# Optimization experiments

Measured on AMD Instinct MI355X. Metric: run time of the kernel, lower is better.

## Reference

```python
import jax, jax.numpy as jnp
import numpy as np

B, S, D, H, L, FF = 32, 512, 256, 8, 2, 512
E = 64  # embed_dim_per_feature
VOCABS = [20, 50, 100]
NCLS = 36
MAX_CONN, THR = 10, 0.6


def _ln(x, g, b, eps=1e-5):
    m = x.mean(-1, keepdims=True)
    v = ((x - m) ** 2).mean(-1, keepdims=True)
    return g * (x - m) / jnp.sqrt(v + eps) + b


def _build_adj(cat, cnt):
    # self loops + chain links + banded similarity links (create_mutation_graph_optimized)
    Bb, _, Ss = cat.shape
    adj = jnp.broadcast_to(jnp.eye(Ss, dtype=jnp.float32), (Bb, Ss, Ss))
    for d in range(1, MAX_CONN):
        if d >= Ss:
            break
        cat_sim = (cat[:, :, :-d] == cat[:, :, d:]).astype(jnp.float32).mean(1)
        cnt_sim = jnp.exp(-jnp.abs(cnt[:, :-d] - cnt[:, d:]) / 100.0)
        sim = 0.5 * (cat_sim + cnt_sim)  # [B, S-d]
        base = 1.0 if d == 1 else 0.0  # chain link stays 1 when sim<=thr
        val = jnp.where(sim > THR, sim, base)
        ii = jnp.arange(Ss - d)
        adj = adj.at[:, ii, ii + d].set(val)
        adj = adj.at[:, ii + d, ii].set(val)
    return adj


def setup_inputs():
    key = jax.random.key(0)
    ks = iter(jax.random.split(key, 40))
    def nrm(shape, s=0.02):
        return jax.random.normal(next(ks), shape, jnp.float32) * s
    return {
        "categorical_x": jax.random.randint(next(ks), (B, 3, S), 0, min(VOCABS)),
        "count_x": jax.random.uniform(next(ks), (B, S), jnp.float32) * 100.0,
        "emb0": nrm((VOCABS[0], E)), "emb1": nrm((VOCABS[1], E)), "emb2": nrm((VOCABS[2], E)),
        "cnt_W": nrm((1, E)), "cnt_b": jnp.zeros((E,), jnp.float32),
        "pos_enc": nrm((S, D)),
        "gat_W": nrm((L, D, D)), "gat_a": nrm((L, 2 * D, 1)),
        "qkv_W": nrm((L, 3 * D, D)), "qkv_b": jnp.zeros((L, 3 * D), jnp.float32),
        "outp_W": nrm((L, D, D)), "outp_b": jnp.zeros((L, D), jnp.float32),
        "ff1_W": nrm((L, FF, D)), "ff1_b": jnp.zeros((L, FF), jnp.float32),
        "ff2_W": nrm((L, D, FF)), "ff2_b": jnp.zeros((L, D), jnp.float32),
        "ln_g": jnp.ones((L, 3, D), jnp.float32), "ln_b": jnp.zeros((L, 3, D), jnp.float32),
        "cls1_W": nrm((D // 2, D)), "cls1_b": jnp.zeros((D // 2,), jnp.float32),
        "cls2_W": nrm((NCLS, D // 2)), "cls2_b": jnp.zeros((NCLS,), jnp.float32),
    }


def reference(categorical_x, count_x, emb0, emb1, emb2, cnt_W, cnt_b, pos_enc,
              gat_W, gat_a, qkv_W, qkv_b, outp_W, outp_b,
              ff1_W, ff1_b, ff2_W, ff2_b, ln_g, ln_b,
              cls1_W, cls1_b, cls2_W, cls2_b):
    Ss = categorical_x.shape[2]
    # per-timestep feature embedding + count projection, concat -> d_model
    x = jnp.concatenate([
        emb0[categorical_x[:, 0]], emb1[categorical_x[:, 1]], emb2[categorical_x[:, 2]],
        count_x[..., None] @ cnt_W + cnt_b], -1)
    x = x + pos_enc[:Ss]
    mask = _build_adj(categorical_x, count_x) > 0  # adj used only as mask
    dh = D // H
    for l in range(L):
        # GraphAttentionLayer: e_ij = Wh_i.a1 + Wh_j.a2 (same math as repeat+concat+matmul)
        Wh = x @ gat_W[l]
        e = (Wh @ gat_a[l][:D, 0])[:, :, None] + (Wh @ gat_a[l][D:, 0])[:, None, :]
        att = jax.nn.softmax(jnp.where(mask, e, -9e15), -1)
        g = jax.nn.elu(att @ Wh)
        x = _ln(x + g, ln_g[l, 0], ln_b[l, 0])
        # MultiheadAttention (batch_first, eval)
        qkv = x @ qkv_W[l].T + qkv_b[l]
        q, k, v = jnp.split(qkv, 3, -1)
        q = q.reshape(-1, Ss, H, dh)
        k = k.reshape(-1, Ss, H, dh)
        v = v.reshape(-1, Ss, H, dh)
        sc = jnp.einsum('bihd,bjhd->bhij', q, k) / jnp.sqrt(jnp.float32(dh))
        o = jnp.einsum('bhij,bjhd->bihd', jax.nn.softmax(sc, -1), v).reshape(-1, Ss, D)
        o = o @ outp_W[l].T + outp_b[l]
        x = _ln(x + o, ln_g[l, 1], ln_b[l, 1])
        # FFN
        ff = jax.nn.relu(x @ ff1_W[l].T + ff1_b[l]) @ ff2_W[l].T + ff2_b[l]
        x = _ln(x + ff, ln_g[l, 2], ln_b[l, 2])
    pooled = x.mean(1)
    h = jax.nn.relu(pooled @ cls1_W.T + cls1_b)
    return h @ cls2_W.T + cls2_b
```

## Files before the change

### kernel.cpp

```cpp
#include <hip/hip_runtime.h>
#include <hip/hip_bf16.h>
#include <math.h>

#define Bn 32
#define Sn 512
#define Dn 256
#define Hn 8
#define DHn 32
#define En 64
#define FFn 512
#define Ln 2
#define NCLSn 36
#define BANDR 9
#define NBn 19
#define Mn (Bn * Sn)

typedef __attribute__((ext_vector_type(8))) short s8v;
typedef __attribute__((ext_vector_type(4))) float f4v;
typedef __attribute__((ext_vector_type(4))) unsigned short us4;
typedef unsigned short ushortT;

__device__ __forceinline__ ushortT f2b(float f) {
    unsigned u = __float_as_uint(f);
    unsigned r = (u + 0x7FFFu + ((u >> 16) & 1u)) >> 16;
    return (ushortT)r;
}

#define GLDS16(g, l)                                                            \
    __builtin_amdgcn_global_load_lds(                                           \
        (const __attribute__((address_space(1))) void*)(g),                     \
        (__attribute__((address_space(3))) void*)(l), 16, 0, 0)

__global__ void k_f2b_all(const float* __restrict__ qkvW, const float* __restrict__ outpW,
                          const float* __restrict__ ff1W, const float* __restrict__ ff2W,
                          const float* __restrict__ gatW,
                          ushortT* __restrict__ qkvWb, ushortT* __restrict__ outpWb,
                          ushortT* __restrict__ ff1Wb, ushortT* __restrict__ ff2Wb,
                          ushortT* __restrict__ gatWb) {
    int bid = blockIdx.x;
    if (bid < 1024) {
        int i4 = bid * 256 + threadIdx.x;
        const float* src; ushortT* dst; int off;
        if (i4 < 98304)       { src = qkvW;  dst = qkvWb;  off = 0; }
        else if (i4 < 131072) { src = outpW; dst = outpWb; off = 98304; }
        else if (i4 < 196608) { src = ff1W;  dst = ff1Wb;  off = 131072; }
        else                  { src = ff2W;  dst = ff2Wb;  off = 196608; }
        int j = (i4 - off) * 4;
        float4 v = *(const float4*)(src + j);
        us4 o = {f2b(v.x), f2b(v.y), f2b(v.z), f2b(v.w)};
        *(us4*)(dst + j) = o;
    } else {
        int i = (bid - 1024) * 256 + threadIdx.x;
        int l = i >> 16, rem = i & 65535;
        int k = rem >> 8, n = rem & 255;
        gatWb[(l << 16) + n * 256 + k] = f2b(gatW[i]);
    }
}

__global__ void k_embed_mask(const int* __restrict__ cat, const float* __restrict__ cnt,
                             const float* __restrict__ e0, const float* __restrict__ e1,
                             const float* __restrict__ e2,
                             const float* __restrict__ cW, const float* __restrict__ cb,
                             const float* __restrict__ pos, float* __restrict__ x,
                             ushortT* __restrict__ xb, unsigned char* __restrict__ maskp) {
    if (blockIdx.x < Mn) {
        int bs = blockIdx.x;
        int d = threadIdx.x;
        int b = bs >> 9, s = bs & 511;
        float v;
        if (d < 64)       v = e0[cat[(b * 3 + 0) * Sn + s] * En + d];
        else if (d < 128) v = e1[cat[(b * 3 + 1) * Sn + s] * En + (d - 64)];
        else if (d < 192) v = e2[cat[(b * 3 + 2) * Sn + s] * En + (d - 128)];
        else              v = cnt[b * Sn + s] * cW[d - 192] + cb[d - 192];
        float y = v + pos[s * Dn + d];
        x[(size_t)bs * Dn + d] = y;
        xb[(size_t)bs * Dn + d] = f2b(y);
    } else {
        int idx = (blockIdx.x - Mn) * 256 + threadIdx.x;
        if (idx >= Bn * Sn * NBn) return;
        int off = idx % NBn;
        int bs = idx / NBn;
        int b = bs >> 9, i = bs & 511;
        int j = i + off - BANDR;
        unsigned char m = 0;
        if (j >= 0 && j < Sn) {
            int dd = off - BANDR;
            int ad = dd < 0 ? -dd : dd;
            if (ad <= 1) {
                m = 1;
            } else {
                int c = 0;
                for (int f = 0; f < 3; f++)
                    c += (cat[(b * 3 + f) * Sn + i] == cat[(b * 3 + f) * Sn + j]);
                float cat_sim = (float)c / 3.0f;
                float cnt_sim = expf(-fabsf(cnt[b * Sn + i] - cnt[b * Sn + j]) / 100.0f);
                float sim = 0.5f * (cat_sim + cnt_sim);
                m = (sim > 0.6f) ? 1 : 0;
            }
        }
        maskp[idx] = m;
    }
}

template <int ACT>
__global__ __launch_bounds__(256) void k_gemm_mfma(const ushortT* __restrict__ A,
                                                   const ushortT* __restrict__ Bt,
                                                   const float* __restrict__ bias,
                                                   ushortT* __restrict__ Cout,
                                                   int M, int N, int K) {
    __shared__ ushortT As[2][128 * 32];
    __shared__ ushortT Bs[2][128 * 32];
    int tid = threadIdx.x;
    int w = tid >> 6, lane = tid & 63;
    int g = lane >> 4, lr = lane & 15;
    int o_ = blockIdx.y * gridDim.x + blockIdx.x;
    int nwg = gridDim.x * gridDim.y;
    int wid = (o_ & 7) * (nwg >> 3) + (o_ >> 3);
    int m0 = (wid / gridDim.x) * 128, n0 = (wid % gridDim.x) * 128;
    int wr = w >> 1, wc = w & 1;
    int NT = K >> 5;
    f4v acc[4][4];
#pragma unroll
    for (int m = 0; m < 4; m++)
#pragma unroll
        for (int n = 0; n < 4; n++) acc[m][n] = (f4v){0.f, 0.f, 0.f, 0.f};

    auto stage = [&](int t, int buf) {
        int k0 = t << 5;
#pragma unroll
        for (int r = 0; r < 2; r++) {
            int e = (tid + r * 256) * 8;
            int row = e >> 5, kk = e & 31;
            GLDS16(A + (size_t)(m0 + row) * K + k0 + kk, &As[buf][e]);
            GLDS16(Bt + (size_t)(n0 + row) * K + k0 + kk, &Bs[buf][e]);
        }
    };

    stage(0, 0);
    __syncthreads();
    for (int t = 0; t < NT; t++) {
        int cur = t & 1;
        if (t + 1 < NT) stage(t + 1, cur ^ 1);
        s8v af[4], bf[4];
#pragma unroll
        for (int m = 0; m < 4; m++)
            af[m] = *(const s8v*)(&As[cur][(wr * 64 + m * 16 + lr) * 32 + g * 8]);
#pragma unroll
        for (int n = 0; n < 4; n++)
            bf[n] = *(const s8v*)(&Bs[cur][(wc * 64 + n * 16 + lr) * 32 + g * 8]);
#pragma unroll
        for (int m = 0; m < 4; m++)
#pragma unroll
            for (int n = 0; n < 4; n++)
                acc[m][n] = __builtin_amdgcn_mfma_f32_16x16x32_bf16(af[m], bf[n], acc[m][n], 0, 0, 0);
        __syncthreads();
    }
#pragma unroll
    for (int m = 0; m < 4; m++) {
#pragma unroll
        for (int n = 0; n < 4; n++) {
            int col = n0 + wc * 64 + n * 16 + lr;
            float bv = bias ? bias[col] : 0.0f;
#pragma unroll
            for (int r = 0; r < 4; r++) {
                int row = m0 + wr * 64 + m * 16 + g * 4 + r;
                float v = acc[m][n][r] + bv;
                if (ACT == 1) v = fmaxf(v, 0.0f);
                Cout[(size_t)row * N + col] = f2b(v);
            }
        }
    }
}

template <int MODE>
__global__ __launch_bounds__(512) void k_gemm_row(const ushortT* __restrict__ A,
                                                  const ushortT* __restrict__ Bt,
                                                  const float* __restrict__ bias,
                                                  const float* __restrict__ ga,
                                                  float* __restrict__ a1h, float* __restrict__ a2h,
                                                  float* __restrict__ Whout,
                                                  const float* __restrict__ lg,
                                                  const float* __restrict__ lb,
                                                  float* __restrict__ x, ushortT* __restrict__ xb,
                                                  int K) {
    __shared__ ushortT As[2][64 * 32];
    __shared__ ushortT Bs[2][256 * 32];
    __shared__ float red1[64][4], red2[64][4];
    int tid = threadIdx.x;
    int w = tid >> 6, lane = tid & 63;
    int g = lane >> 4, lr = lane & 15;
    int wr = w >> 2, wc = w & 3;
    int o_ = blockIdx.x;
    int wid = (o_ & 7) * (gridDim.x >> 3) + (o_ >> 3);
    int m0 = wid * 64;
    int NT = K >> 5;
    f4v acc[2][4];
#pragma unroll
    for (int m = 0; m < 2; m++)
#pragma unroll
        for (int n = 0; n < 4; n++) acc[m][n] = (f4v){0.f, 0.f, 0.f, 0.f};

    auto stage = [&](int t, int buf) {
        int k0 = t << 5;
        if (tid < 256) {
            int e = tid * 8;
            int row = e >> 5, kk = e & 31;
            GLDS16(A + (size_t)(m0 + row) * K + k0 + kk, &As[buf][e]);
        }
#pragma unroll
        for (int r = 0; r < 2; r++) {
            int e = (tid + r * 512) * 8;
            int row = e >> 5, kk = e & 31;
            GLDS16(Bt + (size_t)row * K + k0 + kk, &Bs[buf][e]);
        }
    };

    stage(0, 0);
    __syncthreads();
    for (int t = 0; t < NT; t++) {
        int cur = t & 1;
        if (t + 1 < NT) stage(t + 1, cur ^ 1);
        s8v af[2], bf[4];
#pragma unroll
        for (int m = 0; m < 2; m++)
            af[m] = *(const s8v*)(&As[cur][(wr * 32 + m * 16 + lr) * 32 + g * 8]);
#pragma unroll
        for (int n = 0; n < 4; n++)
            bf[n] = *(const s8v*)(&Bs[cur][(wc * 64 + n * 16 + lr) * 32 + g * 8]);
#pragma unroll
        for (int m = 0; m < 2; m++)
#pragma unroll
            for (int n = 0; n < 4; n++)
                acc[m][n] = __builtin_amdgcn_mfma_f32_16x16x32_bf16(af[m], bf[n], acc[m][n], 0, 0, 0);
        __syncthreads();
    }

    int cn[4];
#pragma unroll
    for (int n = 0; n < 4; n++) cn[n] = wc * 64 + n * 16 + lr;

    if constexpr (MODE == 0) {
        float a1v[4], a2v[4];
#pragma unroll
        for (int n = 0; n < 4; n++) { a1v[n] = ga[cn[n]]; a2v[n] = ga[Dn + cn[n]]; }
#pragma unroll
        for (int m = 0; m < 2; m++)
#pragma unroll
            for (int r = 0; r < 4; r++) {
                int rowl = wr * 32 + m * 16 + g * 4 + r;
                float p1 = 0.f, p2 = 0.f;
#pragma unroll
                for (int n = 0; n < 4; n++) {
                    float v = acc[m][n][r];
                    Whout[(size_t)(m0 + rowl) * Dn + cn[n]] = v;
                    p1 += v * a1v[n];
                    p2 += v * a2v[n];
                }
                p1 += __shfl_xor(p1, 1); p2 += __shfl_xor(p2, 1);
                p1 += __shfl_xor(p1, 2); p2 += __shfl_xor(p2, 2);
                p1 += __shfl_xor(p1, 4); p2 += __shfl_xor(p2, 4);
                p1 += __shfl_xor(p1, 8); p2 += __shfl_xor(p2, 8);
                if (lr == 0) { red1[rowl][wc] = p1; red2[rowl][wc] = p2; }
            }
        __syncthreads();
        if (tid < 64) {
            float t1 = red1[tid][0] + red1[tid][1] + red1[tid][2] + red1[tid][3];
            float t2 = red2[tid][0] + red2[tid][1] + red2[tid][2] + red2[tid][3];
            a1h[m0 + tid] = t1;
            a2h[m0 + tid] = t2;
        }
    } else {
        float bv[4], lgv[4], lbv[4];
#pragma unroll
        for (int n = 0; n < 4; n++) { bv[n] = bias[cn[n]]; lgv[n] = lg[cn[n]]; lbv[n] = lb[cn[n]]; }
#pragma unroll
        for (int m = 0; m < 2; m++)
#pragma unroll
            for (int r = 0; r < 4; r++) {
                int rowl = wr * 32 + m * 16 + g * 4 + r;
                float s1 = 0.f, s2 = 0.f;
#pragma unroll
                for (int n = 0; n < 4; n++) {
                    float y = acc[m][n][r] + bv[n] + x[(size_t)(m0 + rowl) * Dn + cn[n]];
                    acc[m][n][r] = y;
                    s1 += y;
                    s2 += y * y;
                }
                s1 += __shfl_xor(s1, 1); s2 += __shfl_xor(s2, 1);
                s1 += __shfl_xor(s1, 2); s2 += __shfl_xor(s2, 2);
                s1 += __shfl_xor(s1, 4); s2 += __shfl_xor(s2, 4);
                s1 += __shfl_xor(s1, 8); s2 += __shfl_xor(s2, 8);
                if (lr == 0) { red1[rowl][wc] = s1; red2[rowl][wc] = s2; }
            }
        __syncthreads();
#pragma unroll
        for (int m = 0; m < 2; m++)
#pragma unroll
            for (int r = 0; r < 4; r++) {
                int rowl = wr * 32 + m * 16 + g * 4 + r;
                float S1 = red1[rowl][0] + red1[rowl][1] + red1[rowl][2] + red1[rowl][3];
                float S2 = red2[rowl][0] + red2[rowl][1] + red2[rowl][2] + red2[rowl][3];
                float mean = S1 * (1.0f / Dn);
                float var = S2 * (1.0f / Dn) - mean * mean;
                float rs = rsqrtf(var + 1e-5f);
#pragma unroll
                for (int n = 0; n < 4; n++) {
                    float o = lgv[n] * (acc[m][n][r] - mean) * rs + lbv[n];
                    size_t idx = (size_t)(m0 + rowl) * Dn + cn[n];
                    x[idx] = o;
                    xb[idx] = f2b(o);
                }
            }
    }
}

__global__ __launch_bounds__(256) void k_gat_attn_ln(const float* __restrict__ Wh,
                                                     const float* __restrict__ a1h,
                                                     const float* __restrict__ a2h,
                                                     const unsigned char* __restrict__ mask,
                                                     const float* __restrict__ lg,
                                                     const float* __restrict__ lb,
                                                     float* __restrict__ x,
                                                     ushortT* __restrict__ xb) {
    int w = threadIdx.x >> 6, l = threadIdx.x & 63;
    int bs = blockIdx.x * 4 + w;
    int b = bs >> 9, i = bs & 511;
    float e = -1e30f;
    int j = i + l - BANDR;
    if (l < NBn && j >= 0 && j < Sn && mask[bs * NBn + l])
        e = a1h[bs] + a2h[(b << 9) + j];
    float mx = e;
#pragma unroll
    for (int o = 32; o; o >>= 1) mx = fmaxf(mx, __shfl_xor(mx, o));
    float p = (e > -1e29f) ? __expf(e - mx) : 0.0f;
    float sum = p;
#pragma unroll
    for (int o = 32; o; o >>= 1) sum += __shfl_xor(sum, o);
    p *= (1.0f / sum);
    int c4 = l * 4;
    const float* whb = Wh + (size_t)(b << 9) * Dn + c4;
    float gx = 0.f, gy = 0.f, gz = 0.f, gw = 0.f;
#pragma unroll
    for (int o = 0; o < NBn; o++) {
        float wo = __shfl(p, o);
        int jo = i + o - BANDR;
        jo = jo < 0 ? 0 : (jo > Sn - 1 ? Sn - 1 : jo);
        float4 v = *(const float4*)(whb + (size_t)jo * Dn);
        gx += wo * v.x; gy += wo * v.y; gz += wo * v.z; gw += wo * v.w;
    }
    gx = gx > 0.f ? gx : expm1f(gx);
    gy = gy > 0.f ? gy : expm1f(gy);
    gz = gz > 0.f ? gz : expm1f(gz);
    gw = gw > 0.f ? gw : expm1f(gw);
    float4 xv = *(const float4*)(x + (size_t)bs * Dn + c4);
    float y0 = xv.x + gx, y1 = xv.y + gy, y2 = xv.z + gz, y3 = xv.w + gw;
    float s1 = y0 + y1 + y2 + y3;
    float s2 = y0 * y0 + y1 * y1 + y2 * y2 + y3 * y3;
#pragma unroll
    for (int o = 32; o; o >>= 1) {
        s1 += __shfl_xor(s1, o);
        s2 += __shfl_xor(s2, o);
    }
    float mean = s1 * (1.0f / Dn);
    float var = s2 * (1.0f / Dn) - mean * mean;
    float r = rsqrtf(var + 1e-5f);
    float4 lgv = *(const float4*)(lg + c4);
    float4 lbv = *(const float4*)(lb + c4);
    float o0 = lgv.x * (y0 - mean) * r + lbv.x;
    float o1 = lgv.y * (y1 - mean) * r + lbv.y;
    float o2 = lgv.z * (y2 - mean) * r + lbv.z;
    float o3 = lgv.w * (y3 - mean) * r + lbv.w;
    *(float4*)(x + (size_t)bs * Dn + c4) = make_float4(o0, o1, o2, o3);
    us4 ob = {f2b(o0), f2b(o1), f2b(o2), f2b(o3)};
    *(us4*)(xb + (size_t)bs * Dn + c4) = ob;
}

__global__ __launch_bounds__(256) void k_attn_mfma(const ushortT* __restrict__ qkv,
                                                   ushortT* __restrict__ ob) {
    __shared__ ushortT Ks[2][64 * 32];
    __shared__ ushortT Vt[2][32 * 64];
    __shared__ ushortT Ps[4][32 * 72];
    int tid = threadIdx.x;
    int w = tid >> 6, lane = tid & 63;
    int g = lane >> 4, lr = lane & 15;
    int o_ = blockIdx.x;
    int blk = (o_ & 7) * (gridDim.x >> 3) + (o_ >> 3);
    int qq = blk & 3, h = (blk >> 2) & 7, b = blk >> 5;
    const ushortT* base = qkv + (size_t)b * Sn * 768;
    const ushortT* kbase = base + 256 + h * 32;
    const ushortT* vbase = base + 512 + h * 32;

    int krow2 = tid >> 3;
    int kc = (tid & 7) ^ (krow2 & 7);
    int kkv = krow2 * 2 + (kc >> 2);
    int kdd = (kc & 3) * 8;
    int vd0 = w * 8;

    int q0 = qq * 128 + w * 32;
    s8v qf[2];
#pragma unroll
    for (int m = 0; m < 2; m++)
        qf[m] = *(const s8v*)(base + (size_t)(q0 + m * 16 + lr) * 768 + h * 32 + g * 8);

    f4v o[2][2];
    float rl[2][4];
#pragma unroll
    for (int m = 0; m < 2; m++) {
        o[m][0] = (f4v){0.f, 0.f, 0.f, 0.f};
        o[m][1] = (f4v){0.f, 0.f, 0.f, 0.f};
#pragma unroll
        for (int r = 0; r < 4; r++) rl[m][r] = 0.f;
    }
    const float scale2 = 0.25506973f;

    {
        GLDS16(kbase + (size_t)kkv * 768 + kdd, &Ks[0][tid * 8]);
        us4 v0 = *(const us4*)(vbase + (size_t)lane * 768 + vd0);
        us4 v1 = *(const us4*)(vbase + (size_t)lane * 768 + vd0 + 4);
#pragma unroll
        for (int jj = 0; jj < 4; jj++) {
            int d = vd0 + jj;
            Vt[0][d * 64 + (lane ^ ((d & 7) << 3))] = v0[jj];
            int d2 = d + 4;
            Vt[0][d2 * 64 + (lane ^ ((d2 & 7) << 3))] = v1[jj];
        }
    }
    __syncthreads();

    for (int kt = 0; kt < 8; kt++) {
        int cur = kt & 1, nxt = cur ^ 1;
        us4 v0, v1;
        if (kt < 7) {
            GLDS16(kbase + (size_t)((kt + 1) * 64 + kkv) * 768 + kdd, &Ks[nxt][tid * 8]);
            v0 = *(const us4*)(vbase + (size_t)((kt + 1) * 64 + lane) * 768 + vd0);
            v1 = *(const us4*)(vbase + (size_t)((kt + 1) * 64 + lane) * 768 + vd0 + 4);
        }
        s8v kf[4];
#pragma unroll
        for (int n = 0; n < 4; n++) {
            int row2 = n * 8 + (lr >> 1);
            int cc = (((lr & 1) << 2) + g) ^ (row2 & 7);
            kf[n] = *(const s8v*)(&Ks[cur][row2 * 64 + cc * 8]);
        }
        s8v vf[2][2];
#pragma unroll
        for (int cd = 0; cd < 2; cd++)
#pragma unroll
            for (int c2 = 0; c2 < 2; c2++) {
                int d = cd * 16 + lr;
                vf[cd][c2] = *(const s8v*)(&Vt[cur][d * 64 + ((c2 * 32 + g * 8) ^ ((d & 7) << 3))]);
            }
        f4v s[2][4];
#pragma unroll
        for (int m = 0; m < 2; m++)
#pragma unroll
            for (int n = 0; n < 4; n++) {
                f4v z = (f4v){0.f, 0.f, 0.f, 0.f};
                s[m][n] = __builtin_amdgcn_mfma_f32_16x16x32_bf16(qf[m], kf[n], z, 0, 0, 0);
            }
#pragma unroll
        for (int m = 0; m < 2; m++)
#pragma unroll
            for (int r = 0; r < 4; r++) {
                float p0 = exp2f(fminf(s[m][0][r] * scale2, 86.f));
                float p1 = exp2f(fminf(s[m][1][r] * scale2, 86.f));
                float p2 = exp2f(fminf(s[m][2][r] * scale2, 86.f));
                float p3 = exp2f(fminf(s[m][3][r] * scale2, 86.f));
                rl[m][r] += (p0 + p1) + (p2 + p3);
                int rr = m * 16 + g * 4 + r;
                Ps[w][rr * 72 + lr]      = f2b(p0);
                Ps[w][rr * 72 + 16 + lr] = f2b(p1);
                Ps[w][rr * 72 + 32 + lr] = f2b(p2);
                Ps[w][rr * 72 + 48 + lr] = f2b(p3);
            }
#pragma unroll
        for (int m = 0; m < 2; m++) {
            s8v pf0 = *(const s8v*)(&Ps[w][(m * 16 + lr) * 72 + g * 8]);
            s8v pf1 = *(const s8v*)(&Ps[w][(m * 16 + lr) * 72 + 32 + g * 8]);
            o[m][0] = __builtin_amdgcn_mfma_f32_16x16x32_bf16(pf0, vf[0][0], o[m][0], 0, 0, 0);
            o[m][0] = __builtin_amdgcn_mfma_f32_16x16x32_bf16(pf1, vf[0][1], o[m][0], 0, 0, 0);
            o[m][1] = __builtin_amdgcn_mfma_f32_16x16x32_bf16(pf0, vf[1][0], o[m][1], 0, 0, 0);
            o[m][1] = __builtin_amdgcn_mfma_f32_16x16x32_bf16(pf1, vf[1][1], o[m][1], 0, 0, 0);
        }
        if (kt < 7) {
#pragma unroll
            for (int jj = 0; jj < 4; jj++) {
                int d = vd0 + jj;
                Vt[nxt][d * 64 + (lane ^ ((d & 7) << 3))] = v0[jj];
                int d2 = d + 4;
                Vt[nxt][d2 * 64 + (lane ^ ((d2 & 7) << 3))] = v1[jj];
            }
        }
        __syncthreads();
    }
#pragma unroll
    for (int m = 0; m < 2; m++) {
#pragma unroll
        for (int r = 0; r < 4; r++) {
            float t = rl[m][r];
            t += __shfl_xor(t, 1);
            t += __shfl_xor(t, 2);
            t += __shfl_xor(t, 4);
            t += __shfl_xor(t, 8);
            float inv = 1.0f / t;
            int qr = q0 + m * 16 + g * 4 + r;
            size_t obase = ((size_t)(b * Sn + qr)) * Dn + h * 32;
            ob[obase + lr] = f2b(o[m][0][r] * inv);
            ob[obase + 16 + lr] = f2b(o[m][1][r] * inv);
        }
    }
}

__global__ void k_pool_cls(const float* __restrict__ x, const float* __restrict__ w1,
                           const float* __restrict__ b1, const float* __restrict__ w2,
                           const float* __restrict__ b2, float* __restrict__ out) {
    int b = blockIdx.x;
    int t = threadIdx.x;
    __shared__ float pooled[Dn];
    __shared__ float hbuf[128];
    float s = 0.f;
    const float* xp = x + (size_t)(b << 9) * Dn + t;
    for (int sx = 0; sx < Sn; sx++) s += xp[(size_t)sx * Dn];
    pooled[t] = s * (1.0f / Sn);
    __syncthreads();
    if (t < 128) {
        float a = b1[t];
        for (int k = 0; k < Dn; k++) a += pooled[k] * w1[t * Dn + k];
        hbuf[t] = fmaxf(a, 0.0f);
    }
    __syncthreads();
    if (t < NCLSn) {
        float a2 = b2[t];
        for (int k = 0; k < 128; k++) a2 += hbuf[k] * w2[t * 128 + k];
        out[b * NCLSn + t] = a2;
    }
}

extern "C" void kernel_launch(void* const* d_in, const int* in_sizes, int n_in,
                              void* d_out, int out_size, void* d_ws, size_t ws_size,
                              hipStream_t stream) {
    const int* cat = (const int*)d_in[0];
    const float* cnt = (const float*)d_in[1];
    const float* emb0 = (const float*)d_in[2];
    const float* emb1 = (const float*)d_in[3];
    const float* emb2 = (const float*)d_in[4];
    const float* cnt_W = (const float*)d_in[5];
    const float* cnt_b = (const float*)d_in[6];
    const float* pos_enc = (const float*)d_in[7];
    const float* gat_W = (const float*)d_in[8];
    const float* gat_a = (const float*)d_in[9];
    const float* qkv_W = (const float*)d_in[10];
    const float* qkv_b = (const float*)d_in[11];
    const float* outp_W = (const float*)d_in[12];
    const float* outp_b = (const float*)d_in[13];
    const float* ff1_W = (const float*)d_in[14];
    const float* ff1_b = (const float*)d_in[15];
    const float* ff2_W = (const float*)d_in[16];
    const float* ff2_b = (const float*)d_in[17];
    const float* ln_g = (const float*)d_in[18];
    const float* ln_b = (const float*)d_in[19];
    const float* cls1_W = (const float*)d_in[20];
    const float* cls1_b = (const float*)d_in[21];
    const float* cls2_W = (const float*)d_in[22];
    const float* cls2_b = (const float*)d_in[23];
    float* out = (float*)d_out;

    char* wp = (char*)d_ws;
    float* x = (float*)wp;        wp += (size_t)Mn * Dn * 4;
    float* tmpf = (float*)wp;     wp += (size_t)Mn * Dn * 4;
    ushortT* xb = (ushortT*)wp;   wp += (size_t)Mn * Dn * 2;
    ushortT* qkvb = (ushortT*)wp; wp += (size_t)Mn * 3 * Dn * 2;
    ushortT* ffb = qkvb;
    ushortT* obb = (ushortT*)wp;  wp += (size_t)Mn * Dn * 2;
    float* a1h = (float*)wp;      wp += (size_t)Mn * 4;
    float* a2h = (float*)wp;      wp += (size_t)Mn * 4;
    unsigned char* mask = (unsigned char*)wp; wp += (size_t)Mn * NBn;
    ushortT* gatWb = (ushortT*)wp;  wp += (size_t)Ln * Dn * Dn * 2;
    ushortT* qkvWb = (ushortT*)wp;  wp += (size_t)Ln * 3 * Dn * Dn * 2;
    ushortT* outpWb = (ushortT*)wp; wp += (size_t)Ln * Dn * Dn * 2;
    ushortT* ff1Wb = (ushortT*)wp;  wp += (size_t)Ln * FFn * Dn * 2;
    ushortT* ff2Wb = (ushortT*)wp;  wp += (size_t)Ln * Dn * FFn * 2;

    k_f2b_all<<<1536, 256, 0, stream>>>(qkv_W, outp_W, ff1_W, ff2_W, gat_W,
                                        qkvWb, outpWb, ff1Wb, ff2Wb, gatWb);
    k_embed_mask<<<Mn + 1216, 256, 0, stream>>>(cat, cnt, emb0, emb1, emb2, cnt_W, cnt_b,
                                                pos_enc, x, xb, mask);

    for (int l = 0; l < Ln; l++) {
        k_gemm_row<0><<<Mn / 64, 512, 0, stream>>>(
            xb, gatWb + (size_t)l * Dn * Dn, nullptr,
            gat_a + (size_t)l * 2 * Dn, a1h, a2h, tmpf,
            nullptr, nullptr, nullptr, nullptr, Dn);
        k_gat_attn_ln<<<Mn / 4, 256, 0, stream>>>(tmpf, a1h, a2h, mask,
                                                  ln_g + (l * 3 + 0) * Dn, ln_b + (l * 3 + 0) * Dn, x, xb);
        k_gemm_mfma<0><<<dim3(3 * Dn / 128, Mn / 128), 256, 0, stream>>>(
            xb, qkvWb + (size_t)l * 3 * Dn * Dn, qkv_b + l * 3 * Dn, qkvb, Mn, 3 * Dn, Dn);
        k_attn_mfma<<<Bn * Hn * 4, 256, 0, stream>>>(qkvb, obb);
        k_gemm_row<1><<<Mn / 64, 512, 0, stream>>>(
            obb, outpWb + (size_t)l * Dn * Dn, outp_b + l * Dn,
            nullptr, nullptr, nullptr, nullptr,
            ln_g + (l * 3 + 1) * Dn, ln_b + (l * 3 + 1) * Dn, x, xb, Dn);
        k_gemm_mfma<1><<<dim3(FFn / 128, Mn / 128), 256, 0, stream>>>(
            xb, ff1Wb + (size_t)l * FFn * Dn, ff1_b + l * FFn, ffb, Mn, FFn, Dn);
        k_gemm_row<1><<<Mn / 64, 512, 0, stream>>>(
            ffb, ff2Wb + (size_t)l * Dn * FFn, ff2_b + l * Dn,
            nullptr, nullptr, nullptr, nullptr,
            ln_g + (l * 3 + 2) * Dn, ln_b + (l * 3 + 2) * Dn, x, xb, FFn);
    }

    k_pool_cls<<<Bn, 256, 0, stream>>>(x, cls1_W, cls1_b, cls2_W, cls2_b, out);
}
```

Measured before the change: 321.5 us.

## Retile row GEMMs and attention, drop workgroup swizzles, switch softmax to expf

Row-GEMM/LayerNorm blocks go from 64 rows and 512 threads to 32 rows and 256 threads, doubling the grid so each block re-stages the full 256-wide weight tile for fewer rows. Attention blocks now cover 256 queries (64 per wave) instead of 128, halving the grid and K/V reloads, at the cost of more registers per wave. The XCD-style block-index swizzles are removed from all GEMM and attention kernels, and the exp2f with prescaled log2e is replaced by __expf with the plain scale. These changes trade L2 locality and occupancy against K/V reuse and a smaller grid.

```diff
diff --git a/kernel.cpp b/kernel.cpp
--- a/kernel.cpp
+++ b/kernel.cpp
@@ -113,10 +113,7 @@
     int tid = threadIdx.x;
     int w = tid >> 6, lane = tid & 63;
     int g = lane >> 4, lr = lane & 15;
-    int o_ = blockIdx.y * gridDim.x + blockIdx.x;
-    int nwg = gridDim.x * gridDim.y;
-    int wid = (o_ & 7) * (nwg >> 3) + (o_ >> 3);
-    int m0 = (wid / gridDim.x) * 128, n0 = (wid % gridDim.x) * 128;
+    int m0 = blockIdx.y * 128, n0 = blockIdx.x * 128;
     int wr = w >> 1, wc = w & 1;
     int NT = K >> 5;
     f4v acc[4][4];
@@ -173,7 +170,7 @@
 }
 
 template <int MODE>
-__global__ __launch_bounds__(512) void k_gemm_row(const ushortT* __restrict__ A,
+__global__ __launch_bounds__(256) void k_gemm_row(const ushortT* __restrict__ A,
                                                   const ushortT* __restrict__ Bt,
                                                   const float* __restrict__ bias,
                                                   const float* __restrict__ ga,
@@ -183,16 +180,13 @@
                                                   const float* __restrict__ lb,
                                                   float* __restrict__ x, ushortT* __restrict__ xb,
                                                   int K) {
-    __shared__ ushortT As[2][64 * 32];
+    __shared__ ushortT As[2][32 * 32];
     __shared__ ushortT Bs[2][256 * 32];
-    __shared__ float red1[64][4], red2[64][4];
+    __shared__ float red1[32][4], red2[32][4];
     int tid = threadIdx.x;
     int w = tid >> 6, lane = tid & 63;
     int g = lane >> 4, lr = lane & 15;
-    int wr = w >> 2, wc = w & 3;
-    int o_ = blockIdx.x;
-    int wid = (o_ & 7) * (gridDim.x >> 3) + (o_ >> 3);
-    int m0 = wid * 64;
+    int m0 = blockIdx.x * 32;
     int NT = K >> 5;
     f4v acc[2][4];
 #pragma unroll
@@ -202,14 +196,14 @@
 
     auto stage = [&](int t, int buf) {
         int k0 = t << 5;
-        if (tid < 256) {
+        if (tid < 128) {
             int e = tid * 8;
             int row = e >> 5, kk = e & 31;
             GLDS16(A + (size_t)(m0 + row) * K + k0 + kk, &As[buf][e]);
         }
 #pragma unroll
-        for (int r = 0; r < 2; r++) {
-            int e = (tid + r * 512) * 8;
+        for (int r = 0; r < 4; r++) {
+            int e = (tid + r * 256) * 8;
             int row = e >> 5, kk = e & 31;
             GLDS16(Bt + (size_t)row * K + k0 + kk, &Bs[buf][e]);
         }
@@ -223,10 +217,10 @@
         s8v af[2], bf[4];
 #pragma unroll
         for (int m = 0; m < 2; m++)
-            af[m] = *(const s8v*)(&As[cur][(wr * 32 + m * 16 + lr) * 32 + g * 8]);
+            af[m] = *(const s8v*)(&As[cur][(m * 16 + lr) * 32 + g * 8]);
 #pragma unroll
         for (int n = 0; n < 4; n++)
-            bf[n] = *(const s8v*)(&Bs[cur][(wc * 64 + n * 16 + lr) * 32 + g * 8]);
+            bf[n] = *(const s8v*)(&Bs[cur][(w * 64 + n * 16 + lr) * 32 + g * 8]);
 #pragma unroll
         for (int m = 0; m < 2; m++)
 #pragma unroll
@@ -237,7 +231,7 @@
 
     int cn[4];
 #pragma unroll
-    for (int n = 0; n < 4; n++) cn[n] = wc * 64 + n * 16 + lr;
+    for (int n = 0; n < 4; n++) cn[n] = w * 64 + n * 16 + lr;
 
     if constexpr (MODE == 0) {
         float a1v[4], a2v[4];
@@ -247,7 +241,7 @@
         for (int m = 0; m < 2; m++)
 #pragma unroll
             for (int r = 0; r < 4; r++) {
-                int rowl = wr * 32 + m * 16 + g * 4 + r;
+                int rowl = m * 16 + g * 4 + r;
                 float p1 = 0.f, p2 = 0.f;
 #pragma unroll
                 for (int n = 0; n < 4; n++) {
@@ -260,10 +254,10 @@
                 p1 += __shfl_xor(p1, 2); p2 += __shfl_xor(p2, 2);
                 p1 += __shfl_xor(p1, 4); p2 += __shfl_xor(p2, 4);
                 p1 += __shfl_xor(p1, 8); p2 += __shfl_xor(p2, 8);
-                if (lr == 0) { red1[rowl][wc] = p1; red2[rowl][wc] = p2; }
+                if (lr == 0) { red1[rowl][w] = p1; red2[rowl][w] = p2; }
             }
         __syncthreads();
-        if (tid < 64) {
+        if (tid < 32) {
             float t1 = red1[tid][0] + red1[tid][1] + red1[tid][2] + red1[tid][3];
             float t2 = red2[tid][0] + red2[tid][1] + red2[tid][2] + red2[tid][3];
             a1h[m0 + tid] = t1;
@@ -277,7 +271,7 @@
         for (int m = 0; m < 2; m++)
 #pragma unroll
             for (int r = 0; r < 4; r++) {
-                int rowl = wr * 32 + m * 16 + g * 4 + r;
+                int rowl = m * 16 + g * 4 + r;
                 float s1 = 0.f, s2 = 0.f;
 #pragma unroll
                 for (int n = 0; n < 4; n++) {
@@ -290,14 +284,14 @@
                 s1 += __shfl_xor(s1, 2); s2 += __shfl_xor(s2, 2);
                 s1 += __shfl_xor(s1, 4); s2 += __shfl_xor(s2, 4);
                 s1 += __shfl_xor(s1, 8); s2 += __shfl_xor(s2, 8);
-                if (lr == 0) { red1[rowl][wc] = s1; red2[rowl][wc] = s2; }
+                if (lr == 0) { red1[rowl][w] = s1; red2[rowl][w] = s2; }
             }
         __syncthreads();
 #pragma unroll
         for (int m = 0; m < 2; m++)
 #pragma unroll
             for (int r = 0; r < 4; r++) {
-                int rowl = wr * 32 + m * 16 + g * 4 + r;
+                int rowl = m * 16 + g * 4 + r;
                 float S1 = red1[rowl][0] + red1[rowl][1] + red1[rowl][2] + red1[rowl][3];
                 float S2 = red2[rowl][0] + red2[rowl][1] + red2[rowl][2] + red2[rowl][3];
                 float mean = S1 * (1.0f / Dn);
@@ -379,13 +373,12 @@
                                                    ushortT* __restrict__ ob) {
     __shared__ ushortT Ks[2][64 * 32];
     __shared__ ushortT Vt[2][32 * 64];
-    __shared__ ushortT Ps[4][32 * 72];
+    __shared__ ushortT Ps[4][16 * 72];
     int tid = threadIdx.x;
     int w = tid >> 6, lane = tid & 63;
     int g = lane >> 4, lr = lane & 15;
-    int o_ = blockIdx.x;
-    int blk = (o_ & 7) * (gridDim.x >> 3) + (o_ >> 3);
-    int qq = blk & 3, h = (blk >> 2) & 7, b = blk >> 5;
+    int blk = blockIdx.x;
+    int qh = blk & 1, h = (blk >> 1) & 7, b = blk >> 4;
     const ushortT* base = qkv + (size_t)b * Sn * 768;
     const ushortT* kbase = base + 256 + h * 32;
     const ushortT* vbase = base + 512 + h * 32;
@@ -396,22 +389,22 @@
     int kdd = (kc & 3) * 8;
     int vd0 = w * 8;
 
-    int q0 = qq * 128 + w * 32;
-    s8v qf[2];
-#pragma unroll
-    for (int m = 0; m < 2; m++)
+    int q0 = qh * 256 + w * 64;
+    s8v qf[4];
+#pragma unroll
+    for (int m = 0; m < 4; m++)
         qf[m] = *(const s8v*)(base + (size_t)(q0 + m * 16 + lr) * 768 + h * 32 + g * 8);
 
-    f4v o[2][2];
-    float rl[2][4];
-#pragma unroll
-    for (int m = 0; m < 2; m++) {
+    f4v o[4][2];
+    float rl[4][4];
+#pragma unroll
+    for (int m = 0; m < 4; m++) {
         o[m][0] = (f4v){0.f, 0.f, 0.f, 0.f};
         o[m][1] = (f4v){0.f, 0.f, 0.f, 0.f};
 #pragma unroll
         for (int r = 0; r < 4; r++) rl[m][r] = 0.f;
     }
-    const float scale2 = 0.25506973f;
+    const float scale = 0.17677669529663687f;
 
     {
         GLDS16(kbase + (size_t)kkv * 768 + kdd, &Ks[0][tid * 8]);
@@ -450,33 +443,29 @@
                 int d = cd * 16 + lr;
                 vf[cd][c2] = *(const s8v*)(&Vt[cur][d * 64 + ((c2 * 32 + g * 8) ^ ((d & 7) << 3))]);
             }
-        f4v s[2][4];
-#pragma unroll
-        for (int m = 0; m < 2; m++)
+#pragma unroll
+        for (int m = 0; m < 4; m++) {
+            f4v s[4];
 #pragma unroll
             for (int n = 0; n < 4; n++) {
                 f4v z = (f4v){0.f, 0.f, 0.f, 0.f};
-                s[m][n] = __builtin_amdgcn_mfma_f32_16x16x32_bf16(qf[m], kf[n], z, 0, 0, 0);
-            }
-#pragma unroll
-        for (int m = 0; m < 2; m++)
+                s[n] = __builtin_amdgcn_mfma_f32_16x16x32_bf16(qf[m], kf[n], z, 0, 0, 0);
+            }
 #pragma unroll
             for (int r = 0; r < 4; r++) {
-                float p0 = exp2f(fminf(s[m][0][r] * scale2, 86.f));
-                float p1 = exp2f(fminf(s[m][1][r] * scale2, 86.f));
-                float p2 = exp2f(fminf(s[m][2][r] * scale2, 86.f));
-                float p3 = exp2f(fminf(s[m][3][r] * scale2, 86.f));
+                float p0 = __expf(fminf(s[0][r] * scale, 60.f));
+                float p1 = __expf(fminf(s[1][r] * scale, 60.f));
+                float p2 = __expf(fminf(s[2][r] * scale, 60.f));
+                float p3 = __expf(fminf(s[3][r] * scale, 60.f));
                 rl[m][r] += (p0 + p1) + (p2 + p3);
-                int rr = m * 16 + g * 4 + r;
+                int rr = g * 4 + r;
                 Ps[w][rr * 72 + lr]      = f2b(p0);
                 Ps[w][rr * 72 + 16 + lr] = f2b(p1);
                 Ps[w][rr * 72 + 32 + lr] = f2b(p2);
                 Ps[w][rr * 72 + 48 + lr] = f2b(p3);
             }
-#pragma unroll
-        for (int m = 0; m < 2; m++) {
-            s8v pf0 = *(const s8v*)(&Ps[w][(m * 16 + lr) * 72 + g * 8]);
-            s8v pf1 = *(const s8v*)(&Ps[w][(m * 16 + lr) * 72 + 32 + g * 8]);
+            s8v pf0 = *(const s8v*)(&Ps[w][lr * 72 + g * 8]);
+            s8v pf1 = *(const s8v*)(&Ps[w][lr * 72 + 32 + g * 8]);
             o[m][0] = __builtin_amdgcn_mfma_f32_16x16x32_bf16(pf0, vf[0][0], o[m][0], 0, 0, 0);
             o[m][0] = __builtin_amdgcn_mfma_f32_16x16x32_bf16(pf1, vf[0][1], o[m][0], 0, 0, 0);
             o[m][1] = __builtin_amdgcn_mfma_f32_16x16x32_bf16(pf0, vf[1][0], o[m][1], 0, 0, 0);
@@ -494,7 +483,7 @@
         __syncthreads();
     }
 #pragma unroll
-    for (int m = 0; m < 2; m++) {
+    for (int m = 0; m < 4; m++) {
 #pragma unroll
         for (int r = 0; r < 4; r++) {
             float t = rl[m][r];
@@ -587,7 +576,7 @@
                                                 pos_enc, x, xb, mask);
 
     for (int l = 0; l < Ln; l++) {
-        k_gemm_row<0><<<Mn / 64, 512, 0, stream>>>(
+        k_gemm_row<0><<<Mn / 32, 256, 0, stream>>>(
             xb, gatWb + (size_t)l * Dn * Dn, nullptr,
             gat_a + (size_t)l * 2 * Dn, a1h, a2h, tmpf,
             nullptr, nullptr, nullptr, nullptr, Dn);
@@ -595,14 +584,14 @@
                                                   ln_g + (l * 3 + 0) * Dn, ln_b + (l * 3 + 0) * Dn, x, xb);
         k_gemm_mfma<0><<<dim3(3 * Dn / 128, Mn / 128), 256, 0, stream>>>(
             xb, qkvWb + (size_t)l * 3 * Dn * Dn, qkv_b + l * 3 * Dn, qkvb, Mn, 3 * Dn, Dn);
-        k_attn_mfma<<<Bn * Hn * 4, 256, 0, stream>>>(qkvb, obb);
-        k_gemm_row<1><<<Mn / 64, 512, 0, stream>>>(
+        k_attn_mfma<<<Bn * Hn * 2, 256, 0, stream>>>(qkvb, obb);
+        k_gemm_row<1><<<Mn / 32, 256, 0, stream>>>(
             obb, outpWb + (size_t)l * Dn * Dn, outp_b + l * Dn,
             nullptr, nullptr, nullptr, nullptr,
             ln_g + (l * 3 + 1) * Dn, ln_b + (l * 3 + 1) * Dn, x, xb, Dn);
         k_gemm_mfma<1><<<dim3(FFn / 128, Mn / 128), 256, 0, stream>>>(
             xb, ff1Wb + (size_t)l * FFn * Dn, ff1_b + l * FFn, ffb, Mn, FFn, Dn);
-        k_gemm_row<1><<<Mn / 64, 512, 0, stream>>>(
+        k_gemm_row<1><<<Mn / 32, 256, 0, stream>>>(
             ffb, ff2Wb + (size_t)l * Dn * FFn, ff2_b + l * Dn,
             nullptr, nullptr, nullptr, nullptr,
             ln_g + (l * 3 + 2) * Dn, ln_b + (l * 3 + 2) * Dn, x, xb, FFn);
```

Result: faster. 315.1 us (-2.0%).
